# Kernel optimization log

Hardware: AMD Instinct MI355X
Metric: run time of the kernel (lower is better)

## Reference

```python
import jax, jax.numpy as jnp
import numpy as np

# yolov5 non_max_suppression defaults (from forward's input_parameters.get defaults)
CONF_THRES = 0.25
IOU_THRES = 0.45
MAX_DET = 1000        # max detections returned per image
TOP_K = 4096          # fixed candidate count entering greedy NMS (jit-friendly stand-in for max_nms)
MAX_WH = 7680.0       # per-class box offset so NMS is class-aware (yolov5 trick)


def setup_inputs() -> dict:
    key = jax.random.key(0)
    k1, k2, k3, k4 = jax.random.split(key, 4)
    B, N, NC = 16, 25200, 80  # 640x640 yolov5 -> 25200 anchors, 80 COCO classes
    xy = jax.random.uniform(k1, (B, N, 2)) * 640.0            # box centers in pixels
    wh = jax.random.uniform(k2, (B, N, 2)) * 160.0 + 4.0       # box sizes
    obj = jax.random.uniform(k3, (B, N, 1))                    # objectness
    cls = jax.random.uniform(k4, (B, N, NC))                   # class scores
    pred = jnp.concatenate([xy, wh, obj, cls], axis=-1)        # [B, N, 85]
    return {"pred": pred}


def _xywh2xyxy(x):
    xy, wh = x[..., :2], x[..., 2:4]
    return jnp.concatenate([xy - wh * 0.5, xy + wh * 0.5], axis=-1)


def _iou_one_vs_all(box, boxes):
    # box [4], boxes [K,4], xyxy
    lt = jnp.maximum(box[:2], boxes[:, :2])
    rb = jnp.minimum(box[2:], boxes[:, 2:])
    wh = jnp.clip(rb - lt, 0.0)
    inter = wh[:, 0] * wh[:, 1]
    a1 = (box[2] - box[0]) * (box[3] - box[1])
    a2 = (boxes[:, 2] - boxes[:, 0]) * (boxes[:, 3] - boxes[:, 1])
    return inter / (a1 + a2 - inter + 1e-7)


def _nms_single(pred):
    # pred [N, 5+nc] raw yolov5 output for one image
    obj = pred[:, 4:5]
    scores_all = pred[:, 5:] * obj                 # conf = obj_conf * cls_conf
    conf = scores_all.max(axis=-1)                 # best-class confidence [N]
    cls = scores_all.argmax(axis=-1).astype(pred.dtype)
    boxes = _xywh2xyxy(pred[:, :4])                # [N,4] xyxy

    valid = conf > CONF_THRES
    s = jnp.where(valid, conf, -1.0)
    order = jnp.argsort(-s)[:TOP_K]                # top candidates by score
    b = boxes[order]                               # [K,4]
    sc = s[order]                                  # [K]
    c = cls[order]                                 # [K]
    ob = b + c[:, None] * MAX_WH                   # class-offset boxes for class-aware NMS

    ar = jnp.arange(TOP_K)

    def step(supp, i):
        alive = (~supp[i]) & (sc[i] > 0.0)
        iou = _iou_one_vs_all(ob[i], ob)
        supp = supp | (alive & (iou > IOU_THRES) & (ar > i))
        return supp, alive

    _, keep = jax.lax.scan(step, jnp.zeros(TOP_K, dtype=bool), ar)

    fs = jnp.where(keep, sc, -1.0)
    idx = jnp.argsort(-fs)[:MAX_DET]               # kept boxes, score-sorted
    det = jnp.concatenate([b[idx], fs[idx][:, None], c[idx][:, None]], axis=-1)  # [max_det,6]
    ok = fs[idx] > 0.0
    return jnp.where(ok[:, None], det, 0.0)        # zero-padded [max_det, 6] (x1,y1,x2,y2,conf,cls)


def reference(pred):
    # [B, max_det, 6] padded detections per image
    return jax.vmap(_nms_single)(pred)
```

## Files before the change

kernel.cpp:

```cpp
#include <hip/hip_runtime.h>

#define BATCH  16
#define NPRED  25200
#define NCLS   80
#define CDIM   85
#define TOPK   4096
#define NBUCK  4096
#define MAXDET 1000
#define CONF_T 0.25f
#define IOU_T  0.45f
#define MAXWH  7680.0f
#define ORD_BASE 0xBE800000u

typedef unsigned long long u64;
typedef unsigned int u32;
typedef unsigned short u16;
typedef unsigned char u8;

__device__ __forceinline__ u64 umax64(u64 a, u64 b) { return a > b ? a : b; }
__device__ __forceinline__ u64 umin64(u64 a, u64 b) { return a < b ? a : b; }

__device__ __forceinline__ void cx_u64(u64* a, int i, int p, bool desc) {
    u64 x = a[i], y = a[p];
    if (desc ? (x < y) : (x > y)) { a[i] = y; a[p] = x; }
}

__device__ __forceinline__ float4 build_box(const float* __restrict__ row, float off) {
    float x = row[0], y = row[1], w = row[2], hh = row[3];
    float4 o;
    o.x = (x - w * 0.5f) + off;
    o.y = (y - hh * 0.5f) + off;
    o.z = (x + w * 0.5f) + off;
    o.w = (y + hh * 0.5f) + off;
    return o;
}


__device__ void hybrid_sort4096_desc_ks(u64 r[4], u64* a, int kstart) {
    const int tid = threadIdx.x;
    for (int k = kstart; k <= 4096; k <<= 1) {
        if (k >= 512) {
            int jmax = (k >> 1) > 2048 ? 2048 : (k >> 1);
#pragma unroll
            for (int e = 0; e < 4; ++e) a[4 * tid + e] = r[e];
            __syncthreads();
            for (int j = jmax; j >= 256; j >>= 1) {
#pragma unroll
                for (int t2 = 0; t2 < 2; ++t2) {
                    int q = (t2 << 10) | tid;
                    int i = ((q & ~(j - 1)) << 1) | (q & (j - 1));
                    cx_u64(a, i, i | j, (i & k) == 0);
                }
                __syncthreads();
            }
#pragma unroll
            for (int e = 0; e < 4; ++e) r[e] = a[4 * tid + e];
            __syncthreads();
        }
        {
            int jstart = (k >> 1) > 128 ? 128 : (k >> 1);
            bool desc = (((4 * tid) & k) == 0);
            for (int j = jstart; j >= 4; j >>= 1) {
                int m = j >> 2;
                bool take_max = (((tid & m) == 0) == desc);
#pragma unroll
                for (int e = 0; e < 4; ++e) {
                    u64 v = __shfl_xor(r[e], m, 64);
                    r[e] = take_max ? umax64(r[e], v) : umin64(r[e], v);
                }
            }
        }
        if (k >= 4) {
            bool desc = (((4 * tid) & k) == 0);
            u64 x0 = r[0], x2 = r[2];
            r[0] = desc ? umax64(x0, x2) : umin64(x0, x2);
            r[2] = desc ? umin64(x0, x2) : umax64(x0, x2);
            u64 x1 = r[1], x3 = r[3];
            r[1] = desc ? umax64(x1, x3) : umin64(x1, x3);
            r[3] = desc ? umin64(x1, x3) : umax64(x1, x3);
        }
        {
            bool d01 = (((4 * tid + 0) & k) == 0);
            bool d23 = (((4 * tid + 2) & k) == 0);
            u64 x0 = r[0], x1 = r[1];
            r[0] = d01 ? umax64(x0, x1) : umin64(x0, x1);
            r[1] = d01 ? umin64(x0, x1) : umax64(x0, x1);
            u64 x2 = r[2], x3 = r[3];
            r[2] = d23 ? umax64(x2, x3) : umin64(x2, x3);
            r[3] = d23 ? umin64(x2, x3) : umax64(x2, x3);
        }
    }
}


__device__ void hybrid_sort1024_dir(u64 r[4], u64* a, bool fdesc) {
    const int tid = threadIdx.x;
    for (int k = 2; k <= 1024; k <<= 1) {
        if (k >= 512) {
            int jmax = (k >> 1) > 512 ? 512 : (k >> 1);
#pragma unroll
            for (int e = 0; e < 4; ++e) a[4 * tid + e] = r[e];
            __syncthreads();
            for (int j = jmax; j >= 256; j >>= 1) {
#pragma unroll
                for (int t2 = 0; t2 < 2; ++t2) {
                    int q = (t2 << 8) | tid;
                    int i = ((q & ~(j - 1)) << 1) | (q & (j - 1));
                    cx_u64(a, i, i | j, ((i & k) == 0) == fdesc);
                }
                __syncthreads();
            }
#pragma unroll
            for (int e = 0; e < 4; ++e) r[e] = a[4 * tid + e];
            __syncthreads();
        }
        {
            int jstart = (k >> 1) > 128 ? 128 : (k >> 1);
            bool desc = ((((4 * tid) & k) == 0) == fdesc);
            for (int j = jstart; j >= 4; j >>= 1) {
                int m = j >> 2;
                bool take_max = (((tid & m) == 0) == desc);
#pragma unroll
                for (int e = 0; e < 4; ++e) {
                    u64 v = __shfl_xor(r[e], m, 64);
                    r[e] = take_max ? umax64(r[e], v) : umin64(r[e], v);
                }
            }
        }
        if (k >= 4) {
            bool desc = ((((4 * tid) & k) == 0) == fdesc);
            u64 x0 = r[0], x2 = r[2];
            r[0] = desc ? umax64(x0, x2) : umin64(x0, x2);
            r[2] = desc ? umin64(x0, x2) : umax64(x0, x2);
            u64 x1 = r[1], x3 = r[3];
            r[1] = desc ? umax64(x1, x3) : umin64(x1, x3);
            r[3] = desc ? umin64(x1, x3) : umax64(x1, x3);
        }
        {
            bool d01 = ((((4 * tid + 0) & k) == 0) == fdesc);
            bool d23 = ((((4 * tid + 2) & k) == 0) == fdesc);
            u64 x0 = r[0], x1 = r[1];
            r[0] = d01 ? umax64(x0, x1) : umin64(x0, x1);
            r[1] = d01 ? umin64(x0, x1) : umax64(x0, x1);
            u64 x2 = r[2], x3 = r[3];
            r[2] = d23 ? umax64(x2, x3) : umin64(x2, x3);
            r[3] = d23 ? umin64(x2, x3) : umax64(x2, x3);
        }
    }
}

__device__ void wave_sort256_desc(u64 r[4]) {
    const int lane = threadIdx.x & 63;
    for (int k = 2; k <= 256; k <<= 1) {
        int jstart = (k >> 1) > 128 ? 128 : (k >> 1);
        bool desc = (((4 * lane) & k) == 0);
        for (int j = jstart; j >= 4; j >>= 1) {
            int m = j >> 2;
            bool take_max = (((lane & m) == 0) == desc);
#pragma unroll
            for (int e = 0; e < 4; ++e) {
                u64 v = __shfl_xor(r[e], m, 64);
                r[e] = take_max ? umax64(r[e], v) : umin64(r[e], v);
            }
        }
        if (k >= 4) {
            u64 x0 = r[0], x2 = r[2];
            r[0] = desc ? umax64(x0, x2) : umin64(x0, x2);
            r[2] = desc ? umin64(x0, x2) : umax64(x0, x2);
            u64 x1 = r[1], x3 = r[3];
            r[1] = desc ? umax64(x1, x3) : umin64(x1, x3);
            r[3] = desc ? umin64(x1, x3) : umax64(x1, x3);
        }
        {
            bool d01 = (((4 * lane + 0) & k) == 0);
            bool d23 = (((4 * lane + 2) & k) == 0);
            u64 x0 = r[0], x1 = r[1];
            r[0] = d01 ? umax64(x0, x1) : umin64(x0, x1);
            r[1] = d01 ? umin64(x0, x1) : umax64(x0, x1);
            u64 x2 = r[2], x3 = r[3];
            r[2] = d23 ? umax64(x2, x3) : umin64(x2, x3);
            r[3] = d23 ? umin64(x2, x3) : umax64(x2, x3);
        }
    }
}


__global__ __launch_bounds__(256) void k1_score(const float* __restrict__ pred,
                                                u64* __restrict__ keys) {
    const int lane = threadIdx.x & 63;
    const int l16 = lane & 15;
    const long long gw = (long long)blockIdx.x * 4 + (threadIdx.x >> 6);
    const long long rowIdx = gw * 4 + (lane >> 4);
    const int b = (int)(rowIdx / NPRED);
    const int n = (int)(rowIdx - (long long)b * NPRED);
    const float* row = pred + rowIdx * CDIM;
    float obj = row[4];
    u64 m = 0ull;
#pragma unroll
    for (int k = 0; k < 5; ++k) {
        int c = l16 + 16 * k;
        float v = row[5 + c] * obj;
        u64 mk = ((u64)(__float_as_uint(v) | 0x80000000u) << 32) | (u64)(u32)(NCLS - 1 - c);
        if (mk > m) m = mk;
    }
#pragma unroll
    for (int o = 8; o > 0; o >>= 1) {
        u64 other = __shfl_xor(m, o, 64);
        if (other > m) m = other;
    }
    if (l16 == 0) {
        float best = __uint_as_float((u32)(m >> 32) & 0x7FFFFFFFu);
        int cls = (NCLS - 1) - (int)(m & 0x7Fu);
        float s = (best > CONF_T) ? best : -1.0f;
        u32 u = __float_as_uint(s);
        u32 ord = (u & 0x80000000u) ? ~u : (u | 0x80000000u);
        keys[rowIdx] = ((u64)ord << 32) | ((u64)(u32)(32767 - n) << 7) | (u64)(u32)cls;
    }
}


__global__ __launch_bounds__(1024) void k2a(const u64* __restrict__ keys,
                                            u64* __restrict__ topUn,
                                            u8* __restrict__ keep) {
    __shared__ u64 smem[4096];
    __shared__ u64 side[1024];
    __shared__ u32 hist[4096];
    __shared__ u32 wsum[16];
    __shared__ int sh_T, sh_C1, sh_R, c1pos, sidepos;
    const int b = blockIdx.x;
    const int tid = threadIdx.x;
    const int lane = tid & 63;
    const int wid = tid >> 6;
    const u64 lanelt = (1ull << lane) - 1ull;

#pragma unroll
    for (int e = 0; e < 4; ++e) { smem[4 * tid + e] = 0ull; hist[4 * tid + e] = 0u; }
    side[tid] = 0ull;
    ((u32*)keep)[b * 1024 + tid] = 0u;
    __syncthreads();

    const u64* kb = keys + (long long)b * NPRED;
    for (int it = 0; it < (NPRED + 1023) / 1024; ++it) {
        int n = it * 1024 + tid;
        if (n < NPRED) {
            u32 hi = (u32)(kb[n] >> 32);
            if (hi > ORD_BASE) atomicAdd(&hist[(hi - ORD_BASE - 1u) >> 12], 1u);
        }
    }
    __syncthreads();

    u32 h[4];
    u32 tsum = 0;
#pragma unroll
    for (int e = 0; e < 4; ++e) {
        h[e] = hist[NBUCK - 1 - (4 * tid + e)];
        tsum += h[e];
    }
    u32 inc = tsum;
    for (int o = 1; o < 64; o <<= 1) {
        u32 v = __shfl_up(inc, o, 64);
        if (lane >= o) inc += v;
    }
    if (lane == 63) wsum[wid] = inc;
    __syncthreads();
    if (tid == 0) {
        u32 run = 0;
        for (int i = 0; i < 16; ++i) { u32 t = wsum[i]; wsum[i] = run; run += t; }
        sh_T = -1; sh_C1 = (int)run; sh_R = 0;
        c1pos = 0; sidepos = 0;
    }
    __syncthreads();
    {
        u32 cum = wsum[wid] + (inc - tsum);
#pragma unroll
        for (int e = 0; e < 4; ++e) {
            if (h[e] > 0 && cum < (u32)TOPK && cum + h[e] >= (u32)TOPK) {
                sh_T = NBUCK - 1 - (4 * tid + e);
                sh_C1 = (int)cum;
                sh_R = TOPK - (int)cum;
            }
            cum += h[e];
        }
    }
    __syncthreads();
    const int T = sh_T, C1 = sh_C1, R = sh_R;

    for (int it = 0; it < (NPRED + 1023) / 1024; ++it) {
        int n = it * 1024 + tid;
        bool act = n < NPRED;
        u64 key = act ? kb[n] : 0ull;
        u32 hi = (u32)(key >> 32);
        bool v = act && (hi > ORD_BASE);
        int bt = v ? (int)((hi - ORD_BASE - 1u) >> 12) : -1;
        bool t1 = v && (bt > T);
        bool t2 = v && (bt == T);
        u64 m1 = __ballot(t1), m2 = __ballot(t2);
        int b1 = 0, b2 = 0;
        if (lane == 0) {
            if (m1) b1 = atomicAdd(&c1pos, (int)__popcll(m1));
            if (m2) b2 = atomicAdd(&sidepos, (int)__popcll(m2));
        }
        b1 = __shfl(b1, 0, 64);
        b2 = __shfl(b2, 0, 64);
        if (t1) smem[b1 + __popcll(m1 & lanelt)] = key;
        if (t2) { int s2 = b2 + __popcll(m2 & lanelt); if (s2 < 1024) side[s2] = key; }
    }
    __syncthreads();

    if (R > 0) {
        int cntT = sidepos;
        if (cntT <= 256) {
            if (wid == 0) {
                u64 r[4];
#pragma unroll
                for (int e = 0; e < 4; ++e) r[e] = side[4 * lane + e];
                wave_sort256_desc(r);
#pragma unroll
                for (int e = 0; e < 4; ++e) side[4 * lane + e] = r[e];
            }
        } else {
            for (int k = 2; k <= 1024; k <<= 1) {
                for (int j = k >> 1; j >= 1; j >>= 1) {
                    if (tid < 512) {
                        int q = tid;
                        int i = ((q & ~(j - 1)) << 1) | (q & (j - 1));
                        cx_u64(side, i, i | j, (i & k) == 0);
                    }
                    __syncthreads();
                }
            }
        }
        __syncthreads();
        if (tid < R) smem[C1 + tid] = side[tid];
    }
    __syncthreads();

    for (int i = tid; i < 4096; i += 1024) topUn[(long long)b * TOPK + i] = smem[i];
}


__global__ __launch_bounds__(256) void k2b(u64* __restrict__ topUn) {
    __shared__ u64 a[1024];
    const int tid = threadIdx.x;
    const int s = blockIdx.x & 3;
    const long long base = (long long)blockIdx.x * 1024;
    u64 r[4];
#pragma unroll
    for (int e = 0; e < 4; ++e) r[e] = topUn[base + 4 * tid + e];
    hybrid_sort1024_dir(r, a, (s & 1) == 0);
#pragma unroll
    for (int e = 0; e < 4; ++e) topUn[base + 4 * tid + e] = r[e];
}


__global__ __launch_bounds__(1024) void k2c(const u64* __restrict__ topUn,
                                            u64* __restrict__ topSorted) {
    __shared__ u64 a[4096];
    const int b = blockIdx.x;
    const int tid = threadIdx.x;
    u64 r[4];
#pragma unroll
    for (int e = 0; e < 4; ++e) r[e] = topUn[(long long)b * TOPK + 4 * tid + e];
    hybrid_sort4096_desc_ks(r, a, 2048);
#pragma unroll
    for (int e = 0; e < 4; ++e) topSorted[(long long)b * TOPK + 4 * tid + e] = r[e];
}


__global__ __launch_bounds__(64) void k3_nms(const float* __restrict__ pred,
                                             const u64* __restrict__ topSorted,
                                             u8* __restrict__ keep) {
    const int b = blockIdx.x;
    const int c = blockIdx.y;
    const int lane = threadIdx.x;
    __shared__ u32 list[4096];
    __shared__ u8 suppb[4096];
    const u64* tb = topSorted + (long long)b * TOPK;
    const u64 lanelt = (1ull << lane) - 1ull;

    u32 pos = 0;
    for (int it = 0; it < 64; ++it) {
        u64 key = tb[it * 64 + lane];
        u32 hi = (u32)(key >> 32);
        bool mine = (hi > 0x80000000u) && ((int)(key & 0x7Fu) == c);
        u64 m = __ballot(mine);
        if (mine)
            list[pos + __popcll(m & lanelt)] =
                ((u32)(it * 64 + lane) << 15) | (32767u - (u32)((key >> 7) & 0x7FFFu));
        pos += (u32)__popcll(m);
    }
    const int n = (int)pos;
    if (n == 0) return;
    u8* kb = keep + b * TOPK;
    const float off = (float)c * MAXWH;

    if (n <= 128) {
        u32 r0 = 0, r1 = 0;
        float4 b0 = make_float4(0.0f, 0.0f, 0.0f, 0.0f);
        float4 b1 = make_float4(0.0f, 0.0f, 0.0f, 0.0f);
        if (lane < n) {
            u32 e = list[lane];
            r0 = e >> 15;
            b0 = build_box(pred + ((long long)b * NPRED + (int)(e & 0x7FFFu)) * CDIM, off);
        }
        if (64 + lane < n) {
            u32 e = list[64 + lane];
            r1 = e >> 15;
            b1 = build_box(pred + ((long long)b * NPRED + (int)(e & 0x7FFFu)) * CDIM, off);
        }
        {
#pragma clang fp contract(off)
            float a20 = (b0.z - b0.x) * (b0.w - b0.y);
            float a21 = (b1.z - b1.x) * (b1.w - b1.y);
            u64 rem0 = (n >= 64) ? ~0ull : ((1ull << n) - 1ull);
            u64 rem1 = (n > 64) ? ((n >= 128) ? ~0ull : ((1ull << (n - 64)) - 1ull)) : 0ull;
            u64 keep0 = 0ull, keep1 = 0ull;
            const bool two = (n > 64);
            while (rem0) {
                int ii = __builtin_ctzll(rem0);
                rem0 &= ~(1ull << ii);
                keep0 |= 1ull << ii;
                float bix = __shfl(b0.x, ii, 64);
                float biy = __shfl(b0.y, ii, 64);
                float biz = __shfl(b0.z, ii, 64);
                float biw = __shfl(b0.w, ii, 64);
                float a1  = __shfl(a20, ii, 64);
                {
                    float ltx = fmaxf(bix, b0.x), lty = fmaxf(biy, b0.y);
                    float rbx = fminf(biz, b0.z), rby = fminf(biw, b0.w);
                    float ww = fmaxf(rbx - ltx, 0.0f), hh = fmaxf(rby - lty, 0.0f);
                    float inter = ww * hh;
                    float iou = inter / (((a1 + a20) - inter) + 1e-7f);
                    bool k0 = (iou > IOU_T) && (lane > ii);
                    rem0 &= ~__ballot(k0);
                }
                if (two) {
                    float ltx = fmaxf(bix, b1.x), lty = fmaxf(biy, b1.y);
                    float rbx = fminf(biz, b1.z), rby = fminf(biw, b1.w);
                    float ww = fmaxf(rbx - ltx, 0.0f), hh = fmaxf(rby - lty, 0.0f);
                    float inter = ww * hh;
                    float iou = inter / (((a1 + a21) - inter) + 1e-7f);
                    bool k1 = (iou > IOU_T);
                    rem1 &= ~__ballot(k1);
                }
            }
            while (rem1) {
                int ii = __builtin_ctzll(rem1);
                rem1 &= ~(1ull << ii);
                keep1 |= 1ull << ii;
                float bix = __shfl(b1.x, ii, 64);
                float biy = __shfl(b1.y, ii, 64);
                float biz = __shfl(b1.z, ii, 64);
                float biw = __shfl(b1.w, ii, 64);
                float a1  = __shfl(a21, ii, 64);
                float ltx = fmaxf(bix, b1.x), lty = fmaxf(biy, b1.y);
                float rbx = fminf(biz, b1.z), rby = fminf(biw, b1.w);
                float ww = fmaxf(rbx - ltx, 0.0f), hh = fmaxf(rby - lty, 0.0f);
                float inter = ww * hh;
                float iou = inter / (((a1 + a21) - inter) + 1e-7f);
                bool k1 = (iou > IOU_T) && (lane > ii);
                rem1 &= ~__ballot(k1);
            }
            if ((keep0 >> lane) & 1ull) kb[r0] = 1;
            if ((keep1 >> lane) & 1ull) kb[r1] = 1;
        }
    } else {
        for (int j = lane; j < n; j += 64) suppb[j] = 0;
        __syncthreads();
        volatile u8* supp = suppb;
        {
#pragma clang fp contract(off)
            for (int ii = 0; ii < n; ++ii) {
                if (supp[ii]) continue;
                u32 ei = list[ii];
                int ri = (int)(ei >> 15);
                if (lane == 0) kb[ri] = 1;
                float4 bi = build_box(pred + ((long long)b * NPRED + (int)(ei & 0x7FFFu)) * CDIM, off);
                float a1 = (bi.z - bi.x) * (bi.w - bi.y);
                for (int jj = ii + 1 + lane; jj < n; jj += 64) {
                    u32 ej = list[jj];
                    float4 bj = build_box(pred + ((long long)b * NPRED + (int)(ej & 0x7FFFu)) * CDIM, off);
                    float ltx = fmaxf(bi.x, bj.x), lty = fmaxf(bi.y, bj.y);
                    float rbx = fminf(bi.z, bj.z), rby = fminf(bi.w, bj.w);
                    float ww = fmaxf(rbx - ltx, 0.0f), hh = fmaxf(rby - lty, 0.0f);
                    float inter = ww * hh;
                    float a2 = (bj.z - bj.x) * (bj.w - bj.y);
                    float iou = inter / (((a1 + a2) - inter) + 1e-7f);
                    if (iou > IOU_T) supp[jj] = 1;
                }
                __syncthreads();
            }
        }
    }
}


__global__ __launch_bounds__(256) void k4_out(const float* __restrict__ pred,
                                              const u64* __restrict__ topSorted,
                                              const u8* __restrict__ keep,
                                              float* __restrict__ out) {
    const int b = blockIdx.x;
    const int tid = threadIdx.x;
    __shared__ u64 words[64];
    __shared__ int wpre[64];
    float* outb = out + (long long)b * MAXDET * 6;
    for (int i = tid; i < MAXDET * 6; i += 256) outb[i] = 0.0f;
    const u8* kp = keep + b * 4096;
    if (tid < 64) {
        u64 w = 0ull;
        const u64* k8 = (const u64*)(kp + tid * 64);
#pragma unroll
        for (int q = 0; q < 8; ++q) {
            u64 v = k8[q];
#pragma unroll
            for (int bb = 0; bb < 8; ++bb)
                if ((v >> (8 * bb)) & 0xFFull) w |= 1ull << (q * 8 + bb);
        }
        words[tid] = w;
    }
    __syncthreads();
    if (tid == 0) {
        int run = 0;
        for (int t = 0; t < 64; ++t) { wpre[t] = run; run += __popcll(words[t]); }
    }
    __syncthreads();
    const u64* kb = topSorted + (long long)b * TOPK;
    for (int r = tid; r < 4096; r += 256) {
        int wd = r >> 6;
        if ((words[wd] >> (r & 63)) & 1ull) {
            int pos = wpre[wd] + __popcll(words[wd] & ((1ull << (r & 63)) - 1ull));
            if (pos < MAXDET) {
                u64 key = kb[r];
                u32 hi = (u32)(key >> 32);
                int n = 32767 - (int)((key >> 7) & 0x7FFFu);
                const float* row = pred + ((long long)b * NPRED + n) * CDIM;
                float x = row[0], y = row[1], w2 = row[2], h = row[3];
                float* o = outb + pos * 6;
                o[0] = x - w2 * 0.5f;
                o[1] = y - h * 0.5f;
                o[2] = x + w2 * 0.5f;
                o[3] = y + h * 0.5f;
                o[4] = __uint_as_float(hi & 0x7FFFFFFFu);
                o[5] = (float)(key & 0x7Fu);
            }
        }
    }
}


extern "C" void kernel_launch(void* const* d_in, const int* in_sizes, int n_in,
                              void* d_out, int out_size, void* d_ws, size_t ws_size,
                              hipStream_t stream) {
    const float* pred = (const float*)d_in[0];
    float* out = (float*)d_out;

    char* ws = (char*)d_ws;
    u64* keys      = (u64*)ws;
    u64* topUn     = (u64*)(ws + 3225600);
    u64* topSorted = (u64*)(ws + 3749888);
    u8*  keep      = (u8*)(ws + 4274176);

    hipLaunchKernelGGL(k1_score, dim3(BATCH * NPRED / 16), dim3(256), 0, stream,
                       pred, keys);
    hipLaunchKernelGGL(k2a, dim3(BATCH), dim3(1024), 0, stream, keys, topUn, keep);
    hipLaunchKernelGGL(k2b, dim3(BATCH * 4), dim3(256), 0, stream, topUn);
    hipLaunchKernelGGL(k2c, dim3(BATCH), dim3(1024), 0, stream, topUn, topSorted);
    hipLaunchKernelGGL(k3_nms, dim3(BATCH, NCLS), dim3(64), 0, stream,
                       pred, topSorted, keep);
    hipLaunchKernelGGL(k4_out, dim3(BATCH), dim3(256), 0, stream, pred, topSorted, keep, out);
}
```

Before: 273.5 us.

## Bucket sorted candidates by class in sort kernel instead of rescanning per NMS block

```diff
diff --git a/kernel.cpp b/kernel.cpp
--- a/kernel.cpp
+++ b/kernel.cpp
@@ -354,43 +354,86 @@
 
 
 __global__ __launch_bounds__(1024) void k2c(const u64* __restrict__ topUn,
-                                            u64* __restrict__ topSorted) {
+                                            u64* __restrict__ topSorted,
+                                            u32* __restrict__ segIdx,
+                                            u32* __restrict__ cntg,
+                                            u32* __restrict__ startg) {
     __shared__ u64 a[4096];
+    __shared__ u32 cnt[NCLS];
+    __shared__ u32 startc[NCLS];
     const int b = blockIdx.x;
     const int tid = threadIdx.x;
+    const int lane = tid & 63;
+    const int wid = tid >> 6;
+    const u64 lanelt = (1ull << lane) - 1ull;
+
     u64 r[4];
 #pragma unroll
     for (int e = 0; e < 4; ++e) r[e] = topUn[(long long)b * TOPK + 4 * tid + e];
     hybrid_sort4096_desc_ks(r, a, 2048);
 #pragma unroll
     for (int e = 0; e < 4; ++e) topSorted[(long long)b * TOPK + 4 * tid + e] = r[e];
+
+    if (tid < NCLS) cnt[tid] = 0u;
+    __syncthreads();
+    u32* arr = (u32*)a;
+#pragma unroll
+    for (int e = 0; e < 4; ++e) {
+        int j = 4 * tid + e;
+        u64 key = r[e];
+        u32 hi = (u32)(key >> 32);
+        u32 v = 0x7Fu;
+        if (hi > 0x80000000u) {
+            u32 np = 32767u - (u32)((key >> 7) & 0x7FFFu);
+            v = (u32)(key & 0x7Fu) | (np << 7);
+            atomicAdd(&cnt[(int)(key & 0x7Fu)], 1u);
+        }
+        arr[j] = v;
+    }
+    __syncthreads();
+    if (tid == 0) {
+        u32 run = 0;
+        for (int c = 0; c < NCLS; ++c) { startc[c] = run; run += cnt[c]; }
+    }
+    __syncthreads();
+
+    {
+        u32 pos0 = startc[wid +  0], pos1 = startc[wid + 16], pos2 = startc[wid + 32],
+            pos3 = startc[wid + 48], pos4 = startc[wid + 64];
+        u32* sg = segIdx + b * TOPK;
+        for (int it = 0; it < 64; ++it) {
+            int j = it * 64 + lane;
+            u32 aj = arr[j];
+            int cc = (int)(aj & 0x7Fu);
+            u32 entry = ((u32)j << 15) | (aj >> 7);
+            u64 m;
+            m = __ballot(cc == wid +  0); if (cc == wid +  0) sg[pos0 + __popcll(m & lanelt)] = entry; pos0 += (u32)__popcll(m);
+            m = __ballot(cc == wid + 16); if (cc == wid + 16) sg[pos1 + __popcll(m & lanelt)] = entry; pos1 += (u32)__popcll(m);
+            m = __ballot(cc == wid + 32); if (cc == wid + 32) sg[pos2 + __popcll(m & lanelt)] = entry; pos2 += (u32)__popcll(m);
+            m = __ballot(cc == wid + 48); if (cc == wid + 48) sg[pos3 + __popcll(m & lanelt)] = entry; pos3 += (u32)__popcll(m);
+            m = __ballot(cc == wid + 64); if (cc == wid + 64) sg[pos4 + __popcll(m & lanelt)] = entry; pos4 += (u32)__popcll(m);
+        }
+    }
+    if (tid < NCLS) {
+        cntg[b * NCLS + tid] = cnt[tid];
+        startg[b * NCLS + tid] = startc[tid];
+    }
 }
 
 
 __global__ __launch_bounds__(64) void k3_nms(const float* __restrict__ pred,
-                                             const u64* __restrict__ topSorted,
+                                             const u32* __restrict__ segIdx,
+                                             const u32* __restrict__ cntg,
+                                             const u32* __restrict__ startg,
                                              u8* __restrict__ keep) {
     const int b = blockIdx.x;
     const int c = blockIdx.y;
     const int lane = threadIdx.x;
-    __shared__ u32 list[4096];
     __shared__ u8 suppb[4096];
-    const u64* tb = topSorted + (long long)b * TOPK;
-    const u64 lanelt = (1ull << lane) - 1ull;
-
-    u32 pos = 0;
-    for (int it = 0; it < 64; ++it) {
-        u64 key = tb[it * 64 + lane];
-        u32 hi = (u32)(key >> 32);
-        bool mine = (hi > 0x80000000u) && ((int)(key & 0x7Fu) == c);
-        u64 m = __ballot(mine);
-        if (mine)
-            list[pos + __popcll(m & lanelt)] =
-                ((u32)(it * 64 + lane) << 15) | (32767u - (u32)((key >> 7) & 0x7FFFu));
-        pos += (u32)__popcll(m);
-    }
-    const int n = (int)pos;
+    const int n = (int)cntg[b * NCLS + c];
     if (n == 0) return;
+    const u32 base = startg[b * NCLS + c];
+    const u32* seg = segIdx + b * TOPK + base;
     u8* kb = keep + b * TOPK;
     const float off = (float)c * MAXWH;
 
@@ -399,12 +442,12 @@
         float4 b0 = make_float4(0.0f, 0.0f, 0.0f, 0.0f);
         float4 b1 = make_float4(0.0f, 0.0f, 0.0f, 0.0f);
         if (lane < n) {
-            u32 e = list[lane];
+            u32 e = seg[lane];
             r0 = e >> 15;
             b0 = build_box(pred + ((long long)b * NPRED + (int)(e & 0x7FFFu)) * CDIM, off);
         }
         if (64 + lane < n) {
-            u32 e = list[64 + lane];
+            u32 e = seg[64 + lane];
             r1 = e >> 15;
             b1 = build_box(pred + ((long long)b * NPRED + (int)(e & 0x7FFFu)) * CDIM, off);
         }
@@ -472,13 +515,13 @@
 #pragma clang fp contract(off)
             for (int ii = 0; ii < n; ++ii) {
                 if (supp[ii]) continue;
-                u32 ei = list[ii];
+                u32 ei = seg[ii];
                 int ri = (int)(ei >> 15);
                 if (lane == 0) kb[ri] = 1;
                 float4 bi = build_box(pred + ((long long)b * NPRED + (int)(ei & 0x7FFFu)) * CDIM, off);
                 float a1 = (bi.z - bi.x) * (bi.w - bi.y);
                 for (int jj = ii + 1 + lane; jj < n; jj += 64) {
-                    u32 ej = list[jj];
+                    u32 ej = seg[jj];
                     float4 bj = build_box(pred + ((long long)b * NPRED + (int)(ej & 0x7FFFu)) * CDIM, off);
                     float ltx = fmaxf(bi.x, bj.x), lty = fmaxf(bi.y, bj.y);
                     float rbx = fminf(bi.z, bj.z), rby = fminf(bi.w, bj.w);
@@ -558,14 +601,18 @@
     u64* keys      = (u64*)ws;
     u64* topUn     = (u64*)(ws + 3225600);
     u64* topSorted = (u64*)(ws + 3749888);
-    u8*  keep      = (u8*)(ws + 4274176);
+    u32* segIdx    = (u32*)(ws + 4274176);
+    u32* cntg      = (u32*)(ws + 4536320);
+    u32* startg    = (u32*)(ws + 4541440);
+    u8*  keep      = (u8*)(ws + 4546560);
 
     hipLaunchKernelGGL(k1_score, dim3(BATCH * NPRED / 16), dim3(256), 0, stream,
                        pred, keys);
     hipLaunchKernelGGL(k2a, dim3(BATCH), dim3(1024), 0, stream, keys, topUn, keep);
     hipLaunchKernelGGL(k2b, dim3(BATCH * 4), dim3(256), 0, stream, topUn);
-    hipLaunchKernelGGL(k2c, dim3(BATCH), dim3(1024), 0, stream, topUn, topSorted);
+    hipLaunchKernelGGL(k2c, dim3(BATCH), dim3(1024), 0, stream, topUn, topSorted,
+                       segIdx, cntg, startg);
     hipLaunchKernelGGL(k3_nms, dim3(BATCH, NCLS), dim3(64), 0, stream,
-                       pred, topSorted, keep);
+                       pred, segIdx, cntg, startg, keep);
     hipLaunchKernelGGL(k4_out, dim3(BATCH), dim3(256), 0, stream, pred, topSorted, keep, out);
 }
```

After: 276.6 us. No clear change (+1.2%).
